# Kernel optimization log

Measured on AMD Instinct MI355X. Metric: run time of the kernel, lower is better.

The kernel has to match this reference:

```python
import jax, jax.numpy as jnp
import numpy as np

B, C, H, W = 32, 256, 56, 56
NUM_ITER = 5

# Row-major upper-triangular (incl. diagonal) flat indices, matching
# torch.ones(C, C).triu().view(-1).nonzero() in the original triuvec.
_r, _c = np.triu_indices(C)
TRIU_IDX = jnp.asarray(_r * C + _c)


def setup_inputs() -> dict:
    key = jax.random.key(0)
    x = jax.random.normal(key, (B, C, H, W), dtype=jnp.float32)
    return {"x": x}


def _cov_pool(x):
    # x: (b, c, h, w) -> sigma = x_n @ ((1/n) I - (1/n^2) J) @ x_n^T : (b, c, c)
    b, c, h, w = x.shape
    n = h * w
    xn = x.reshape(b, c, n)
    s = xn.sum(axis=2)  # (b, c) = x_n @ ones
    gram = jnp.einsum('bcn,bdn->bcd', xn, xn)  # (b, c, c)
    return gram / n - jnp.einsum('bc,bd->bcd', s, s) / (n * n)


def _newton_schulz_sqrt(x, num_iter):
    # x: (b, m, m) SPD; returns approx matrix square root, scaled by sqrt(trace).
    b, m, _ = x.shape
    eye = jnp.eye(m, dtype=x.dtype)
    x_trace = jnp.trace(x, axis1=1, axis2=2)[:, None, None]  # (b, 1, 1)
    a = x / x_trace
    i3 = 3.0 * eye  # broadcasts over batch
    # iteration 0
    b2 = 0.5 * (i3 - a)
    yi = a @ b2
    zi = b2

    def body(carry, _):
        yi, zi = carry
        b2 = 0.5 * (i3 - zi @ yi)
        return (yi @ b2, b2 @ zi), None

    (yi, zi), _ = jax.lax.scan(body, (yi, zi), None, length=num_iter - 1)
    return yi * jnp.sqrt(x_trace)


def _triuvec(x):
    # (b, c, c) -> (b, c*(c+1)//2), row-major upper triangle incl. diagonal
    b, c, _ = x.shape
    return x.reshape(b, c * c)[:, TRIU_IDX]


def reference(x) -> jnp.ndarray:
    cov = _cov_pool(x)
    y = _newton_schulz_sqrt(cov, NUM_ITER)
    return _triuvec(y)
```

## Files before the change

kernel.cpp:

```cpp
#include <hip/hip_runtime.h>
#include <hip/hip_bf16.h>
#include <math.h>

#define BATCH 32
#define C 256
#define HW 3136
#define OUTROW 32896
#define KSPLIT 7
#define KCHUNK 448
#define KC32 98
#define KCG 49
#define SLAB 16384
#define HALF 8192


typedef __bf16 b8v __attribute__((ext_vector_type(8)));
typedef float  f4v __attribute__((ext_vector_type(4)));
typedef unsigned short u16x8 __attribute__((ext_vector_type(8)));

__device__ __forceinline__ unsigned short f2bf(float f) {
    union { float f; unsigned u; } v; v.f = f;
    unsigned r = v.u + 0x7FFFu + ((v.u >> 16) & 1u);
    return (unsigned short)(r >> 16);
}
__device__ __forceinline__ float bf2f(unsigned short h) {
    union { unsigned u; float f; } v; v.u = ((unsigned)h) << 16; return v.f;
}
__device__ __forceinline__ void split2(float x, unsigned short& h, unsigned short& l) {
    h = f2bf(x);
    l = f2bf(x - bf2f(h));
}

__device__ __forceinline__ float wave_sum(float v) {
    for (int o = 32; o; o >>= 1) v += __shfl_down(v, o, 64);
    return v;
}

__global__ __launch_bounds__(256) void k_prep(const float* __restrict__ x,
                                              unsigned short* __restrict__ X,
                                              float* __restrict__ psum,
                                              float* __restrict__ qsum) {
    const int blk = blockIdx.x;
    const int b = blk / KCG;
    const int g = blk - b * KCG;
    const int kc0 = g * 2;
    const int t = threadIdx.x;
    const int lane4 = t & 3;
    const int rowoff = t >> 2;
    const int ko = lane4 * 8;

    const float* xb = x + (size_t)b * C * HW + (size_t)kc0 * 32 + ko;
    unsigned short* s0 = X + (size_t)(b * KC32 + kc0) * SLAB + ko;
    unsigned short* s1 = s0 + SLAB;
    float* ps = psum + (size_t)blk * 256;
    float* qs = qsum + (size_t)blk * 256;

#pragma unroll
    for (int it = 0; it < 4; ++it) {
        const int row = it * 64 + rowoff;
        const float* src = xb + (size_t)row * HW;
        float4 v0 = *(const float4*)(src);
        float4 v1 = *(const float4*)(src + 4);
        float4 v2 = *(const float4*)(src + 32);
        float4 v3 = *(const float4*)(src + 36);
        float va[8] = { v0.x, v0.y, v0.z, v0.w, v1.x, v1.y, v1.z, v1.w };
        float vb[8] = { v2.x, v2.y, v2.z, v2.w, v3.x, v3.y, v3.z, v3.w };
        unsigned short ha[8], la[8], hb[8], lb[8];
        float s = 0.f, q = 0.f;
#pragma unroll
        for (int j = 0; j < 8; ++j) {
            split2(va[j], ha[j], la[j]);
            split2(vb[j], hb[j], lb[j]);
            s += va[j] + vb[j];
            q = fmaf(va[j], va[j], q);
            q = fmaf(vb[j], vb[j], q);
        }
        *(u16x8*)(s0 + row * 32) = *(u16x8*)ha;
        *(u16x8*)(s0 + HALF + row * 32) = *(u16x8*)la;
        *(u16x8*)(s1 + row * 32) = *(u16x8*)hb;
        *(u16x8*)(s1 + HALF + row * 32) = *(u16x8*)lb;
        s += __shfl_xor(s, 1, 64);
        s += __shfl_xor(s, 2, 64);
        q += __shfl_xor(q, 1, 64);
        q += __shfl_xor(q, 2, 64);
        if (lane4 == 0) { ps[row] = s; qs[row] = q; }
    }
}

__global__ __launch_bounds__(256) void k_tr(const float* __restrict__ psum,
                                            const float* __restrict__ qsum,
                                            float* __restrict__ sbuf,
                                            float* __restrict__ trbuf,
                                            float* __restrict__ strbuf) {
    const int b = blockIdx.x, t = threadIdx.x;
    const float* ps = psum + (size_t)b * KCG * 256 + t;
    const float* qs = qsum + (size_t)b * KCG * 256 + t;
    float s = 0.f, q = 0.f;
#pragma unroll 7
    for (int g = 0; g < KCG; ++g) {
        s += ps[(size_t)g * 256];
        q += qs[(size_t)g * 256];
    }
    sbuf[b * C + t] = s;
    const float invn = 1.f / (float)HW, invn2 = invn * invn;
    float v = q * invn - s * s * invn2;
    v = wave_sum(v);
    __shared__ float red[4];
    if ((t & 63) == 0) red[t >> 6] = v;
    __syncthreads();
    if (t == 0) {
        float tr = red[0] + red[1] + red[2] + red[3];
        trbuf[b] = tr;
        strbuf[b] = sqrtf(tr);
    }
}

__global__ __launch_bounds__(64) void k_gram_split(
    const unsigned short* __restrict__ X, float* __restrict__ part) {
    const int bid = blockIdx.x;
    const int x8 = bid & 7;
    const int t8 = bid >> 3;
    const int pairIdx = t8 % 10;
    const int g = (t8 / 10) * 8 + x8;
    const int b = g & 31;
    const int z = g >> 5;

    int p = pairIdx, tm = 0, rem = 4;
    while (p >= rem) { p -= rem; ++tm; --rem; }
    const int tn = tm + p;

    const int lane = threadIdx.x & 63;
    const int q = lane >> 4, r = lane & 15;
    const int kc0 = z * (KCHUNK / 32);
    const size_t matb = (size_t)b * KC32 * SLAB;

    int oA[4], oB[4];
#pragma unroll
    for (int i = 0; i < 4; ++i) {
        oA[i] = (tm * 64 + i * 16 + r) * 32 + q * 8;
        oB[i] = (tn * 64 + i * 16 + r) * 32 + q * 8;
    }

    f4v acc[4][4] = {};
    b8v fAh[2][4], fAl[2][4], fBh[2][4], fBl[2][4];
#define LDG(buf, kc)                                                     \
    do {                                                                 \
        const size_t sb = matb + (size_t)(kc0 + (kc)) * SLAB;            \
        for (int i = 0; i < 4; ++i) {                                    \
            fAh[buf][i] = *(const b8v*)(X + sb + oA[i]);                 \
            fAl[buf][i] = *(const b8v*)(X + sb + HALF + oA[i]);          \
            fBh[buf][i] = *(const b8v*)(X + sb + oB[i]);                 \
            fBl[buf][i] = *(const b8v*)(X + sb + HALF + oB[i]);          \
        }                                                                \
    } while (0)

    LDG(0, 0);
#pragma unroll
    for (int kc = 0; kc < KCHUNK / 32; ++kc) {
        const int cb = kc & 1, nb = cb ^ 1;
        if (kc < KCHUNK / 32 - 1) LDG(nb, kc + 1);
#pragma unroll
        for (int i = 0; i < 4; ++i)
#pragma unroll
            for (int j = 0; j < 4; ++j) {
                acc[i][j] = __builtin_amdgcn_mfma_f32_16x16x32_bf16(fAh[cb][i], fBh[cb][j], acc[i][j], 0, 0, 0);
                acc[i][j] = __builtin_amdgcn_mfma_f32_16x16x32_bf16(fAh[cb][i], fBl[cb][j], acc[i][j], 0, 0, 0);
                acc[i][j] = __builtin_amdgcn_mfma_f32_16x16x32_bf16(fAl[cb][i], fBh[cb][j], acc[i][j], 0, 0, 0);
            }
    }
#undef LDG

    float* pt = part + (((size_t)pairIdx * BATCH + b) * KSPLIT + z) * 4096;
#pragma unroll
    for (int i = 0; i < 4; ++i)
#pragma unroll
        for (int j = 0; j < 4; ++j)
#pragma unroll
            for (int reg = 0; reg < 4; ++reg) {
                int row = i * 16 + q * 4 + reg;
                int col = j * 16 + r;
                pt[row * 64 + col] = acc[i][j][reg];
            }
}

__global__ __launch_bounds__(256) void k_reduce(
    const float* __restrict__ part, const float* __restrict__ sbuf,
    const float* __restrict__ trbuf,
    unsigned short* __restrict__ A, unsigned short* __restrict__ Z) {
    const int b = blockIdx.y;
    int p = blockIdx.x, tm = 0, rem = 4;
    while (p >= rem) { p -= rem; ++tm; --rem; }
    const int tn = tm + p;

    const float* pb = part + ((size_t)blockIdx.x * BATCH + b) * KSPLIT * 4096;
    const int t = threadIdx.x;
    const int row = t >> 2, c0 = (t & 3) * 16;

    float s[16];
#pragma unroll
    for (int u = 0; u < 16; ++u) s[u] = 0.f;
    for (int sp = 0; sp < KSPLIT; ++sp) {
        const float* q4 = pb + sp * 4096 + row * 64 + c0;
#pragma unroll
        for (int u4 = 0; u4 < 4; ++u4) {
            float4 v = *(const float4*)(q4 + u4 * 4);
            s[u4 * 4 + 0] += v.x; s[u4 * 4 + 1] += v.y;
            s[u4 * 4 + 2] += v.z; s[u4 * 4 + 3] += v.w;
        }
    }

    const float invn = 1.f / (float)HW, invn2 = invn * invn;
    const float tr = trbuf[b];
    const int gi = tm * 64 + row;
    const float si = sbuf[b * C + gi];
    const size_t mb = (size_t)b * 8 * SLAB;

    __shared__ unsigned short tAh[64][66], tAl[64][66], tZh[64][66], tZl[64][66];
    unsigned short vAh[16], vAl[16], vZh[16], vZl[16];
#pragma unroll
    for (int u = 0; u < 16; ++u) {
        int gj = tn * 64 + c0 + u;
        float sj = sbuf[b * C + gj];
        float a = (s[u] * invn - si * sj * invn2) / tr;
        split2(a, vAh[u], vAl[u]);
        float zv = ((gi == gj) ? 1.5f : 0.f) - 0.5f * a;
        split2(zv, vZh[u], vZl[u]);
        tAh[row][c0 + u] = vAh[u]; tAl[row][c0 + u] = vAl[u];
        tZh[row][c0 + u] = vZh[u]; tZl[row][c0 + u] = vZl[u];
    }
#pragma unroll
    for (int u4 = 0; u4 < 4; ++u4) {
        const int col0 = tn * 64 + c0 + u4 * 4;
        const size_t off = mb + (size_t)(col0 >> 5) * SLAB + (size_t)gi * 32 + (col0 & 31);
        *(ushort4*)&A[off] = *(ushort4*)&vAh[u4 * 4];
        *(ushort4*)&A[off + HALF] = *(ushort4*)&vAl[u4 * 4];
        *(ushort4*)&Z[off] = *(ushort4*)&vZh[u4 * 4];
        *(ushort4*)&Z[off + HALF] = *(ushort4*)&vZl[u4 * 4];
    }
    if (tm != tn) {
        __syncthreads();
        const int mr = t >> 2, mc0 = (t & 3) * 16;
        const int gim = tn * 64 + mr;
        unsigned short wAh[16], wAl[16], wZh[16], wZl[16];
#pragma unroll
        for (int u = 0; u < 16; ++u) {
            wAh[u] = tAh[mc0 + u][mr]; wAl[u] = tAl[mc0 + u][mr];
            wZh[u] = tZh[mc0 + u][mr]; wZl[u] = tZl[mc0 + u][mr];
        }
#pragma unroll
        for (int u4 = 0; u4 < 4; ++u4) {
            const int col0 = tm * 64 + mc0 + u4 * 4;
            const size_t off = mb + (size_t)(col0 >> 5) * SLAB + (size_t)gim * 32 + (col0 & 31);
            *(ushort4*)&A[off] = *(ushort4*)&wAh[u4 * 4];
            *(ushort4*)&A[off + HALF] = *(ushort4*)&wAl[u4 * 4];
            *(ushort4*)&Z[off] = *(ushort4*)&wZh[u4 * 4];
            *(ushort4*)&Z[off + HALF] = *(ushort4*)&wZl[u4 * 4];
        }
    }
}

__device__ __forceinline__ void wave_gemm64(
    const unsigned short* __restrict__ A, const unsigned short* __restrict__ B,
    int rowA, int rowB, f4v acc[4][4]) {
    const int lane = threadIdx.x & 63;
    const int q = lane >> 4, r = lane & 15;
    int oA[4], oB[4];
#pragma unroll
    for (int i = 0; i < 4; ++i) {
        oA[i] = (rowA + i * 16 + r) * 32 + q * 8;
        oB[i] = (rowB + i * 16 + r) * 32 + q * 8;
    }
    b8v fAh[2][4], fAl[2][4], fBh[2][4], fBl[2][4];
#define LD(buf, kc)                                              \
    do {                                                         \
        const size_t sb = (size_t)(kc) * SLAB;                   \
        for (int i = 0; i < 4; ++i) {                            \
            fAh[buf][i] = *(const b8v*)(A + sb + oA[i]);         \
            fAl[buf][i] = *(const b8v*)(A + sb + HALF + oA[i]);  \
            fBh[buf][i] = *(const b8v*)(B + sb + oB[i]);         \
            fBl[buf][i] = *(const b8v*)(B + sb + HALF + oB[i]);  \
        }                                                        \
    } while (0)

    LD(0, 0);
#pragma unroll
    for (int kc = 0; kc < 8; ++kc) {
        const int cb = kc & 1, nb = cb ^ 1;
        if (kc < 7) LD(nb, kc + 1);
#pragma unroll
        for (int i = 0; i < 4; ++i)
#pragma unroll
            for (int j = 0; j < 4; ++j) {
                acc[i][j] = __builtin_amdgcn_mfma_f32_16x16x32_bf16(fAh[cb][i], fBh[cb][j], acc[i][j], 0, 0, 0);
                acc[i][j] = __builtin_amdgcn_mfma_f32_16x16x32_bf16(fAh[cb][i], fBl[cb][j], acc[i][j], 0, 0, 0);
                acc[i][j] = __builtin_amdgcn_mfma_f32_16x16x32_bf16(fAl[cb][i], fBh[cb][j], acc[i][j], 0, 0, 0);
            }
    }
#undef LD
}

__device__ __forceinline__ void store_tile_fm(
    unsigned short* __restrict__ D, int tm, int tn, const f4v acc[4][4], bool modeT) {
    __shared__ unsigned short lh[64][68];
    __shared__ unsigned short ll[64][68];
    const int lane = threadIdx.x & 63, q = lane >> 4, r = lane & 15;
#pragma unroll
    for (int i = 0; i < 4; ++i)
#pragma unroll
        for (int j = 0; j < 4; ++j) {
            const int col = j * 16 + r;
#pragma unroll
            for (int reg = 0; reg < 4; ++reg) {
                const int row = i * 16 + q * 4 + reg;
                float v = acc[i][j][reg];
                if (modeT) v = ((tm * 64 + row == tn * 64 + col) ? 1.5f : 0.f) - 0.5f * v;
                unsigned short h, l;
                split2(v, h, l);
                lh[row][col] = h;
                ll[row][col] = l;
            }
        }
    __syncthreads();
    const int rowL = lane;
    const size_t gbase = (size_t)(tm * 64 + rowL) * 32;
#pragma unroll
    for (int c = 0; c < 8; ++c) {
        const int gj0 = tn * 64 + c * 8;
        const size_t off = (size_t)(gj0 >> 5) * SLAB + gbase + (gj0 & 31);
        union { ushort4 u4[2]; u16x8 u8; } hv, lv;
        hv.u4[0] = *(const ushort4*)&lh[rowL][c * 8];
        hv.u4[1] = *(const ushort4*)&lh[rowL][c * 8 + 4];
        lv.u4[0] = *(const ushort4*)&ll[rowL][c * 8];
        lv.u4[1] = *(const ushort4*)&ll[rowL][c * 8 + 4];
        *(u16x8*)&D[off] = hv.u8;
        *(u16x8*)&D[off + HALF] = lv.u8;
    }
}

template <int MODE>
__global__ __launch_bounds__(64) void k_t64(
    const unsigned short* __restrict__ A, const unsigned short* __restrict__ B,
    unsigned short* __restrict__ D, float* __restrict__ outF,
    const float* __restrict__ strbuf) {
    const int bid = blockIdx.x;
    const int x8 = bid & 7;
    const int w = bid >> 3;
    int b, tm = 0, tn = 0;
    if (MODE == 2) {
        b = x8 + 8 * (w / 10);
        int p = w % 10, rem = 4;
        while (p >= rem) { p -= rem; ++tm; --rem; }
        tn = tm + p;
    } else {
        b = x8 + 8 * (w >> 4);
        const int tile = w & 15;
        tm = tile >> 2; tn = tile & 3;
    }
    const size_t mo = (size_t)b * 8 * SLAB;
    f4v acc[4][4] = {};
    wave_gemm64(A + mo, B + mo, tm * 64, tn * 64, acc);

    if (MODE == 2) {
        const int lane = threadIdx.x & 63, q = lane >> 4, r = lane & 15;
        const float sc = strbuf[b];
#pragma unroll
        for (int i = 0; i < 4; ++i)
#pragma unroll
            for (int j = 0; j < 4; ++j) {
                const int gj = tn * 64 + j * 16 + r;
#pragma unroll
                for (int reg = 0; reg < 4; ++reg) {
                    const int gi = tm * 64 + i * 16 + q * 4 + reg;
                    if (gj >= gi)
                        outF[(size_t)b * OUTROW + (size_t)(gi * C - (gi * (gi - 1)) / 2) +
                             (gj - gi)] = acc[i][j][reg] * sc;
                }
            }
    } else {
        store_tile_fm(D + mo, tm, tn, acc, MODE == 1);
    }
}

__global__ __launch_bounds__(64) void k_yz64(
    const unsigned short* __restrict__ Y, const unsigned short* __restrict__ T,
    const unsigned short* __restrict__ Z,
    unsigned short* __restrict__ Yn, unsigned short* __restrict__ Zn) {
    const int bid = blockIdx.x;
    const int x8 = bid & 7;
    const int w = bid >> 3;
    const int b = x8 + 8 * ((w >> 4) & 3);
    const int zz = w >> 6;
    const int tile = w & 15;
    const int tm = tile >> 2, tn = tile & 3;

    const unsigned short* Am = zz ? T : Y;
    const unsigned short* Bm = zz ? Z : T;
    unsigned short* Dm = zz ? Zn : Yn;

    const size_t mo = (size_t)b * 8 * SLAB;
    f4v acc[4][4] = {};
    wave_gemm64(Am + mo, Bm + mo, tm * 64, tn * 64, acc);
    store_tile_fm(Dm + mo, tm, tn, acc, false);
}

extern "C" void kernel_launch(void* const* d_in, const int* in_sizes, int n_in,
                              void* d_out, int out_size, void* d_ws, size_t ws_size,
                              hipStream_t stream) {
    const float* x = (const float*)d_in[0];
    float* out = (float*)d_out;

    unsigned short* W = (unsigned short*)d_ws;
    const size_t XS = (size_t)BATCH * KC32 * SLAB;
    const size_t MS = (size_t)BATCH * 8 * SLAB;
    unsigned short* X = W;
    float* sbuf = (float*)(X + XS);
    float* trbuf = sbuf + BATCH * C;
    float* strbuf = trbuf + BATCH;
    unsigned short* P = (unsigned short*)(strbuf + BATCH);
    unsigned short* PA = P + 0 * MS;
    unsigned short* PB = P + 1 * MS;
    unsigned short* PC = P + 2 * MS;
    unsigned short* PD = P + 3 * MS;
    unsigned short* PE = P + 4 * MS;
    float* part = (float*)PC;
    float* psum = (float*)PA;
    float* qsum = psum + (size_t)BATCH * KCG * 256;

    k_prep<<<dim3(BATCH * KCG), 256, 0, stream>>>(x, X, psum, qsum);
    k_tr<<<dim3(BATCH), 256, 0, stream>>>(psum, qsum, sbuf, trbuf, strbuf);
    k_gram_split<<<dim3(10 * BATCH * KSPLIT), 64, 0, stream>>>(X, part);
    k_reduce<<<dim3(10, BATCH), 256, 0, stream>>>(part, sbuf, trbuf, PA, PB);

    dim3 g512(512);
    k_t64<0><<<g512, 64, 0, stream>>>(PA, PB, PC, nullptr, strbuf);
    k_t64<1><<<g512, 64, 0, stream>>>(PB, PC, PD, nullptr, strbuf);
    k_yz64<<<dim3(1024), 64, 0, stream>>>(PC, PD, PB, PA, PE);
    k_t64<1><<<g512, 64, 0, stream>>>(PE, PA, PB, nullptr, strbuf);
    k_yz64<<<dim3(1024), 64, 0, stream>>>(PA, PB, PE, PC, PD);
    k_t64<1><<<g512, 64, 0, stream>>>(PD, PC, PA, nullptr, strbuf);
    k_yz64<<<dim3(1024), 64, 0, stream>>>(PC, PA, PD, PB, PE);
    k_t64<1><<<g512, 64, 0, stream>>>(PE, PB, PC, nullptr, strbuf);
    k_t64<2><<<dim3(320), 64, 0, stream>>>(PB, PC, nullptr, out, strbuf);
}
```

Before: 378.2 us.

## Split K across two waves per 64x64 tile with LDS reduction of halves

Each Newton-Schulz GEMM block now runs two waves, and each wave computes half of the K dimension (4 of 8 slabs). The partial accumulators are exchanged through shared memory so each wave finishes and stores half of the tile's rows. This aims to double wave-level parallelism and shorten the serial MFMA chain in these latency-bound small-grid kernels. In exchange it adds an LDS exchange with a barrier. It also replaces the staged, vectorised LDS store with scattered 2-byte global stores, which may hurt write efficiency.

After: 419.2 us. 10.8% more time.

```diff
diff --git a/kernel.cpp b/kernel.cpp
--- a/kernel.cpp
+++ b/kernel.cpp
@@ -259,9 +259,9 @@
     }
 }
 
-__device__ __forceinline__ void wave_gemm64(
+__device__ __forceinline__ void wave_gemm64h(
     const unsigned short* __restrict__ A, const unsigned short* __restrict__ B,
-    int rowA, int rowB, f4v acc[4][4]) {
+    int rowA, int rowB, int kcBase, f4v acc[4][4]) {
     const int lane = threadIdx.x & 63;
     const int q = lane >> 4, r = lane & 15;
     int oA[4], oB[4];
@@ -273,7 +273,7 @@
     b8v fAh[2][4], fAl[2][4], fBh[2][4], fBl[2][4];
 #define LD(buf, kc)                                              \
     do {                                                         \
-        const size_t sb = (size_t)(kc) * SLAB;                   \
+        const size_t sb = (size_t)(kcBase + (kc)) * SLAB;        \
         for (int i = 0; i < 4; ++i) {                            \
             fAh[buf][i] = *(const b8v*)(A + sb + oA[i]);         \
             fAl[buf][i] = *(const b8v*)(A + sb + HALF + oA[i]);  \
@@ -284,9 +284,9 @@
 
     LD(0, 0);
 #pragma unroll
-    for (int kc = 0; kc < 8; ++kc) {
+    for (int kc = 0; kc < 4; ++kc) {
         const int cb = kc & 1, nb = cb ^ 1;
-        if (kc < 7) LD(nb, kc + 1);
+        if (kc < 3) LD(nb, kc + 1);
 #pragma unroll
         for (int i = 0; i < 4; ++i)
 #pragma unroll
@@ -299,46 +299,48 @@
 #undef LD
 }
 
-__device__ __forceinline__ void store_tile_fm(
-    unsigned short* __restrict__ D, int tm, int tn, const f4v acc[4][4], bool modeT) {
-    __shared__ unsigned short lh[64][68];
-    __shared__ unsigned short ll[64][68];
+__device__ __forceinline__ void exchange_halves(f4v acc[4][4],
+                                                f4v (*xbuf)[2][4][64], int wv) {
+    const int lane = threadIdx.x & 63;
+    const int keep = wv * 2, give = 2 - keep;
+#pragma unroll
+    for (int i2 = 0; i2 < 2; ++i2)
+#pragma unroll
+        for (int j = 0; j < 4; ++j)
+            xbuf[wv][i2][j][lane] = acc[give + i2][j];
+    __syncthreads();
+#pragma unroll
+    for (int i2 = 0; i2 < 2; ++i2)
+#pragma unroll
+        for (int j = 0; j < 4; ++j)
+            acc[keep + i2][j] += xbuf[wv ^ 1][i2][j][lane];
+}
+
+__device__ __forceinline__ void store_half_fm(
+    unsigned short* __restrict__ D, int tm, int tn,
+    const f4v acc[4][4], int keep, bool modeT) {
     const int lane = threadIdx.x & 63, q = lane >> 4, r = lane & 15;
 #pragma unroll
-    for (int i = 0; i < 4; ++i)
+    for (int i2 = 0; i2 < 2; ++i2)
 #pragma unroll
         for (int j = 0; j < 4; ++j) {
-            const int col = j * 16 + r;
+            const int gj = tn * 64 + j * 16 + r;
+            const size_t cbase = (size_t)(gj >> 5) * SLAB + (gj & 31);
 #pragma unroll
             for (int reg = 0; reg < 4; ++reg) {
-                const int row = i * 16 + q * 4 + reg;
-                float v = acc[i][j][reg];
-                if (modeT) v = ((tm * 64 + row == tn * 64 + col) ? 1.5f : 0.f) - 0.5f * v;
+                const int gi = tm * 64 + (keep + i2) * 16 + q * 4 + reg;
+                float v = acc[keep + i2][j][reg];
+                if (modeT) v = ((gi == gj) ? 1.5f : 0.f) - 0.5f * v;
                 unsigned short h, l;
                 split2(v, h, l);
-                lh[row][col] = h;
-                ll[row][col] = l;
+                D[cbase + (size_t)gi * 32] = h;
+                D[cbase + HALF + (size_t)gi * 32] = l;
             }
         }
-    __syncthreads();
-    const int rowL = lane;
-    const size_t gbase = (size_t)(tm * 64 + rowL) * 32;
-#pragma unroll
-    for (int c = 0; c < 8; ++c) {
-        const int gj0 = tn * 64 + c * 8;
-        const size_t off = (size_t)(gj0 >> 5) * SLAB + gbase + (gj0 & 31);
-        union { ushort4 u4[2]; u16x8 u8; } hv, lv;
-        hv.u4[0] = *(const ushort4*)&lh[rowL][c * 8];
-        hv.u4[1] = *(const ushort4*)&lh[rowL][c * 8 + 4];
-        lv.u4[0] = *(const ushort4*)&ll[rowL][c * 8];
-        lv.u4[1] = *(const ushort4*)&ll[rowL][c * 8 + 4];
-        *(u16x8*)&D[off] = hv.u8;
-        *(u16x8*)&D[off + HALF] = lv.u8;
-    }
 }
 
 template <int MODE>
-__global__ __launch_bounds__(64) void k_t64(
+__global__ __launch_bounds__(128) void k_t64(
     const unsigned short* __restrict__ A, const unsigned short* __restrict__ B,
     unsigned short* __restrict__ D, float* __restrict__ outF,
     const float* __restrict__ strbuf) {
@@ -356,32 +358,37 @@
         const int tile = w & 15;
         tm = tile >> 2; tn = tile & 3;
     }
+    const int wv = threadIdx.x >> 6;
     const size_t mo = (size_t)b * 8 * SLAB;
     f4v acc[4][4] = {};
-    wave_gemm64(A + mo, B + mo, tm * 64, tn * 64, acc);
+    wave_gemm64h(A + mo, B + mo, tm * 64, tn * 64, wv * 4, acc);
+
+    __shared__ f4v xbuf[2][2][4][64];
+    exchange_halves(acc, xbuf, wv);
+    const int keep = wv * 2;
 
     if (MODE == 2) {
         const int lane = threadIdx.x & 63, q = lane >> 4, r = lane & 15;
         const float sc = strbuf[b];
 #pragma unroll
-        for (int i = 0; i < 4; ++i)
+        for (int i2 = 0; i2 < 2; ++i2)
 #pragma unroll
             for (int j = 0; j < 4; ++j) {
                 const int gj = tn * 64 + j * 16 + r;
 #pragma unroll
                 for (int reg = 0; reg < 4; ++reg) {
-                    const int gi = tm * 64 + i * 16 + q * 4 + reg;
+                    const int gi = tm * 64 + (keep + i2) * 16 + q * 4 + reg;
                     if (gj >= gi)
                         outF[(size_t)b * OUTROW + (size_t)(gi * C - (gi * (gi - 1)) / 2) +
-                             (gj - gi)] = acc[i][j][reg] * sc;
+                             (gj - gi)] = acc[keep + i2][j][reg] * sc;
                 }
             }
     } else {
-        store_tile_fm(D + mo, tm, tn, acc, MODE == 1);
-    }
-}
-
-__global__ __launch_bounds__(64) void k_yz64(
+        store_half_fm(D + mo, tm, tn, acc, keep, MODE == 1);
+    }
+}
+
+__global__ __launch_bounds__(128) void k_yz64(
     const unsigned short* __restrict__ Y, const unsigned short* __restrict__ T,
     const unsigned short* __restrict__ Z,
     unsigned short* __restrict__ Yn, unsigned short* __restrict__ Zn) {
@@ -397,10 +404,14 @@
     const unsigned short* Bm = zz ? Z : T;
     unsigned short* Dm = zz ? Zn : Yn;
 
+    const int wv = threadIdx.x >> 6;
     const size_t mo = (size_t)b * 8 * SLAB;
     f4v acc[4][4] = {};
-    wave_gemm64(Am + mo, Bm + mo, tm * 64, tn * 64, acc);
-    store_tile_fm(Dm + mo, tm, tn, acc, false);
+    wave_gemm64h(Am + mo, Bm + mo, tm * 64, tn * 64, wv * 4, acc);
+
+    __shared__ f4v xbuf[2][2][4][64];
+    exchange_halves(acc, xbuf, wv);
+    store_half_fm(Dm + mo, tm, tn, acc, wv * 2, false);
 }
 
 extern "C" void kernel_launch(void* const* d_in, const int* in_sizes, int n_in,
@@ -432,13 +443,13 @@
     k_reduce<<<dim3(10, BATCH), 256, 0, stream>>>(part, sbuf, trbuf, PA, PB);
 
     dim3 g512(512);
-    k_t64<0><<<g512, 64, 0, stream>>>(PA, PB, PC, nullptr, strbuf);
-    k_t64<1><<<g512, 64, 0, stream>>>(PB, PC, PD, nullptr, strbuf);
-    k_yz64<<<dim3(1024), 64, 0, stream>>>(PC, PD, PB, PA, PE);
-    k_t64<1><<<g512, 64, 0, stream>>>(PE, PA, PB, nullptr, strbuf);
-    k_yz64<<<dim3(1024), 64, 0, stream>>>(PA, PB, PE, PC, PD);
-    k_t64<1><<<g512, 64, 0, stream>>>(PD, PC, PA, nullptr, strbuf);
-    k_yz64<<<dim3(1024), 64, 0, stream>>>(PC, PA, PD, PB, PE);
-    k_t64<1><<<g512, 64, 0, stream>>>(PE, PB, PC, nullptr, strbuf);
-    k_t64<2><<<dim3(320), 64, 0, stream>>>(PB, PC, nullptr, out, strbuf);
-}
+    k_t64<0><<<g512, 128, 0, stream>>>(PA, PB, PC, nullptr, strbuf);
+    k_t64<1><<<g512, 128, 0, stream>>>(PB, PC, PD, nullptr, strbuf);
+    k_yz64<<<dim3(1024), 128, 0, stream>>>(PC, PD, PB, PA, PE);
+    k_t64<1><<<g512, 128, 0, stream>>>(PE, PA, PB, nullptr, strbuf);
+    k_yz64<<<dim3(1024), 128, 0, stream>>>(PA, PB, PE, PC, PD);
+    k_t64<1><<<g512, 128, 0, stream>>>(PD, PC, PA, nullptr, strbuf);
+    k_yz64<<<dim3(1024), 128, 0, stream>>>(PC, PA, PD, PB, PE);
+    k_t64<1><<<g512, 128, 0, stream>>>(PE, PB, PC, nullptr, strbuf);
+    k_t64<2><<<dim3(320), 128, 0, stream>>>(PB, PC, nullptr, out, strbuf);
+}
```
